# Performance work log

Measured on AMD Instinct MI355X. Metric: run time of the kernel, lower is better.

Reference implementation:

```python
import math
import jax, jax.numpy as jnp
import numpy as np

N_HEAD = 16
ROPE_BASE = 10000.0


def _qk_norm(x, scale):
    # RMSNorm over head_dim, eps added inside sqrt as in the torch code
    norm = jnp.sqrt(jnp.mean(x.astype(jnp.float32) ** 2, axis=-1, keepdims=True) + 1e-6)
    return (x.astype(jnp.float32) / norm * scale).astype(x.dtype)


def _rope3d(q, k, coords, token_type):
    # q,k: [B,H,T,D]; coords: [B,T,3]; token_type: [B,T]
    # head_dim is split into 3 equal chunks, chunk i rotated by coords[...,i].
    # Tokens with token_type == 0 (e.g. text tokens) are left unrotated.
    B, H, T, D = q.shape
    d3 = D // 3
    half = d3 // 2
    inv_freq = ROPE_BASE ** (-jnp.arange(half, dtype=jnp.float32) / half)  # [half]

    def rotate(x):
        # x: [B,H,T,D] -> rotate each of the 3 axis-chunks
        chunks = []
        for a in range(3):
            xa = x[..., a * d3:(a + 1) * d3]                       # [B,H,T,d3]
            ang = coords[:, None, :, a, None] * inv_freq            # [B,1,T,half]
            cos, sin = jnp.cos(ang), jnp.sin(ang)
            x1, x2 = xa[..., :half], xa[..., half:]
            chunks.append(jnp.concatenate([x1 * cos - x2 * sin,
                                           x1 * sin + x2 * cos], axis=-1))
        rot = jnp.concatenate(chunks, axis=-1)
        apply = (token_type > 0)[:, None, :, None]                  # [B,1,T,1]
        return jnp.where(apply, rot, x)

    return rotate(q), rotate(k)


def setup_inputs() -> dict:
    key = jax.random.key(0)
    ks = jax.random.split(key, 5)
    B, T, C = 2, 2048, 1536
    D = C // N_HEAD
    return {
        "x": jax.random.normal(ks[0], (B, T, C), jnp.float32),
        "coords": jax.random.uniform(ks[1], (B, T, 3), jnp.float32) * 32.0,
        "token_type": jax.random.randint(ks[2], (B, T), 0, 2),
        "W_qkv": jax.random.normal(ks[3], (3 * C, C), jnp.float32) * (1.0 / math.sqrt(C)),
        "W_out": jax.random.normal(ks[4], (C, C), jnp.float32) * (1.0 / math.sqrt(C)),
        "q_scale": jnp.ones((D,), jnp.float32),
        "k_scale": jnp.ones((D,), jnp.float32),
    }


def reference(x, coords, token_type, W_qkv, W_out, q_scale, k_scale):
    B, T, C = x.shape
    H = N_HEAD
    D = C // H
    qkv = x @ W_qkv.T                                   # [B,T,3C]
    q, k, v = jnp.split(qkv, 3, axis=-1)
    q = q.reshape(B, T, H, D).transpose(0, 2, 1, 3)     # [B,H,T,D]
    k = k.reshape(B, T, H, D).transpose(0, 2, 1, 3)
    v = v.reshape(B, T, H, D).transpose(0, 2, 1, 3)
    q = _qk_norm(q, q_scale)
    k = _qk_norm(k, k_scale)
    q, k = _rope3d(q, k, coords, token_type)
    scale = 1.0 / math.sqrt(D)
    attn = jnp.einsum('bhqd,bhkd->bhqk', q, k) * scale  # [B,H,T,T]
    causal = jnp.tril(jnp.ones((T, T), bool))
    attn = jnp.where(causal, attn, -jnp.inf)
    attn = jax.nn.softmax(attn, axis=-1)
    out = jnp.einsum('bhqk,bhkd->bhqd', attn, v)        # [B,H,T,D]
    out = out.transpose(0, 2, 1, 3).reshape(B, T, C)
    return out @ W_out.T
```

## Files before the change

### kernel.cpp

```cpp
#include <hip/hip_runtime.h>
#include <stdint.h>
#include <stddef.h>


typedef __attribute__((ext_vector_type(8))) __bf16 bf16x8;
typedef __attribute__((ext_vector_type(4))) __bf16 bf16x4;
typedef __attribute__((ext_vector_type(4))) float  f32x4;

#define NB 2
#define NT 2048
#define NC 1536
#define NH 16
#define ND 96
#define NQKV 4608
#define NM 4096

static __device__ __forceinline__ float fexp2(float x) {
#if __has_builtin(__builtin_amdgcn_exp2f)
  return __builtin_amdgcn_exp2f(x);
#else
  return exp2f(x);
#endif
}

static __device__ __forceinline__ void g2lds16(const void* g, void* l) {
  __builtin_amdgcn_global_load_lds(
      (const __attribute__((address_space(1))) void*)g,
      (__attribute__((address_space(3))) void*)l, 16, 0, 0);
}

__global__ __launch_bounds__(256) void cvt_f32_bf16(
    const float4* __restrict__ src, bf16x4* __restrict__ dst, int n4) {
  int i = blockIdx.x * 256 + threadIdx.x;
  if (i < n4) {
    float4 v = src[i];
    bf16x4 o;
    o[0] = (__bf16)v.x; o[1] = (__bf16)v.y;
    o[2] = (__bf16)v.z; o[3] = (__bf16)v.w;
    dst[i] = o;
  }
}

#define BAR1() do { __builtin_amdgcn_s_barrier(); \
                    asm volatile("" ::: "memory"); } while (0)
#define BAR2() do { asm volatile("" ::: "memory"); \
                    __builtin_amdgcn_s_barrier(); } while (0)
#define WAITLGKM() do { asm volatile("s_waitcnt lgkmcnt(0)" ::: "memory"); \
                        __builtin_amdgcn_sched_barrier(0); } while (0)
#define WAITVM6() asm volatile("s_waitcnt vmcnt(6)" ::: "memory")
#define WAITVM5() asm volatile("s_waitcnt vmcnt(5)" ::: "memory")

template <int MH>
static __device__ __forceinline__ void readA2(
    bf16x8 (&aR)[2][2], const char* buf, int aro, int sk0, int sk1) {
#pragma unroll
  for (int i = 0; i < 2; ++i) {
    const char* p = buf + aro + (MH * 2 + i) * 2048;
    aR[i][0] = *(const bf16x8*)(p + sk0);
    aR[i][1] = *(const bf16x8*)(p + sk1);
  }
}
template <int NF0, int NN>
static __device__ __forceinline__ void readBN(
    bf16x8 (&bb)[NN][2], const char* buf, int bro, int sk0, int sk1) {
#pragma unroll
  for (int j = 0; j < NN; ++j) {
    const char* p = buf + bro + (NF0 + j) * 2048;
    bb[j][0] = *(const bf16x8*)(p + sk0);
    bb[j][1] = *(const bf16x8*)(p + sk1);
  }
}
template <int MH, int NF0, int NN>
static __device__ __forceinline__ void quadN(
    f32x4 (&acc)[4][9], const bf16x8 (&aR)[2][2], const bf16x8 (&bb)[NN][2]) {
  __builtin_amdgcn_s_setprio(1);
#pragma unroll
  for (int i = 0; i < 2; ++i)
#pragma unroll
    for (int j = 0; j < NN; ++j)
#pragma unroll
      for (int ks = 0; ks < 2; ++ks)
        acc[MH * 2 + i][NF0 + j] = __builtin_amdgcn_mfma_f32_16x16x32_bf16(
            aR[i][ks], bb[j][ks], acc[MH * 2 + i][NF0 + j], 0, 0, 0);
  __builtin_amdgcn_s_setprio(0);
}

__global__ __launch_bounds__(512, 2) void gemm1_8ph(
    const __bf16* __restrict__ A, const __bf16* __restrict__ Bw,
    __bf16* __restrict__ C, int M, int N, int K) {
  __shared__ __align__(16) char lds[139264];
  char* const A0 = lds;
  char* const A1 = lds + 32768;
  char* const B0 = lds + 65536;
  char* const B1 = lds + 102400;

  const int tid = threadIdx.x;
  const int l   = tid & 63;
  const int w   = tid >> 6;
  const int wm  = w >> 1;
  const int wn  = w & 1;
  const int lm  = l & 15;
  const int lq  = l >> 4;

  const int nnt = 16;
  const int nwg = gridDim.x * gridDim.y;
  const int lid = blockIdx.y * gridDim.x + blockIdx.x;
  const int swz = (lid & 7) * (nwg >> 3) + (lid >> 3);
  const int m0  = (swz / nnt) * 256;
  const int n0  = (swz % nnt) * 288;

  const int aro = (wm * 64 + lm) * 128;
  const int bro = (wn * 144 + lm) * 128;
  const int sk0 = ((lq) ^ (lm & 7)) * 16;
  const int sk1 = ((4 + lq) ^ (lm & 7)) * 16;

  const int ssl = ((l & 7) ^ ((l >> 3) & 7)) * 8;
  auto stageA = [&](int grow0, int k0, char* dst) {
#pragma unroll
    for (int q2 = 0; q2 < 2; ++q2) {
      const int c   = w * 2 + q2;
      const int row = c * 8 + (l >> 3);
      g2lds16(A + (size_t)(grow0 + row) * K + k0 + ssl, dst + c * 1024);
    }
  };
  auto stageB = [&](int grow0, int k0, char* dst) {
#pragma unroll
    for (int q2 = 0; q2 < 2; ++q2) {
      const int c   = w * 2 + q2;
      const int row = c * 8 + (l >> 3);
      g2lds16(Bw + (size_t)(grow0 + row) * K + k0 + ssl, dst + c * 1024);
    }
    if (w < 2) {
      const int c   = 16 + w;
      const int row = c * 8 + (l >> 3);
      g2lds16(Bw + (size_t)(grow0 + row) * K + k0 + ssl, dst + c * 1024);
    }
  };

  f32x4 acc[4][9] = {};
  bf16x8 aL[2][2], aH[2][2], b5[5][2], b4[4][2];

  stageA(m0,       0,  A0);
  stageA(m0 + 128, 0,  A0 + 16384);
  stageB(n0,       0,  B0);
  stageB(n0 + 144, 0,  B0 + 18432);
  stageA(m0,       64, A1);
  stageA(m0 + 128, 64, A1 + 16384);

  const int NIT = K >> 7;
  for (int it = 0; it < NIT; ++it) {
    const int kh  = it * 128 + 64;
    const int knl = it * 128 + 128;
    const int knh = it * 128 + 192;
    stageB(n0, kh, B1);
    WAITVM6();
    BAR1();
    readA2<0>(aL, A0, aro, sk0, sk1);
    readBN<0, 5>(b5, B0, bro, sk0, sk1);
    WAITLGKM();
    quadN<0, 0, 5>(acc, aL, b5);
    BAR2();
    stageB(n0 + 144, kh, B1 + 18432);
    BAR1();
    readA2<1>(aH, A0, aro, sk0, sk1);
    WAITLGKM();
    quadN<1, 0, 5>(acc, aH, b5);
    BAR2();
    stageA(m0, knl, A0);
    BAR1();
    readBN<5, 4>(b4, B0, bro, sk0, sk1);
    WAITLGKM();
    quadN<1, 5, 4>(acc, aH, b4);
    BAR2();
    stageA(m0 + 128, knl, A0 + 16384);
    BAR1();
    quadN<0, 5, 4>(acc, aL, b4);
    BAR2();
    stageB(n0, knl, B0);
    WAITVM6();
    BAR1();
    readA2<0>(aL, A1, aro, sk0, sk1);
    readBN<0, 5>(b5, B1, bro, sk0, sk1);
    WAITLGKM();
    quadN<0, 0, 5>(acc, aL, b5);
    BAR2();
    stageB(n0 + 144, knl, B0 + 18432);
    BAR1();
    readA2<1>(aH, A1, aro, sk0, sk1);
    WAITLGKM();
    quadN<1, 0, 5>(acc, aH, b5);
    BAR2();
    stageA(m0, knh, A1);
    BAR1();
    readBN<5, 4>(b4, B1, bro, sk0, sk1);
    WAITLGKM();
    quadN<1, 5, 4>(acc, aH, b4);
    BAR2();
    stageA(m0 + 128, knh, A1 + 16384);
    BAR1();
    quadN<0, 5, 4>(acc, aL, b4);
    BAR2();
  }

  const int r0 = lq * 4;
#pragma unroll
  for (int mf = 0; mf < 4; ++mf)
#pragma unroll
    for (int nf = 0; nf < 9; ++nf)
#pragma unroll
      for (int r = 0; r < 4; ++r) {
        const size_t row = (size_t)(m0 + wm * 64 + mf * 16 + r0 + r);
        const size_t col = (size_t)(n0 + wn * 144 + nf * 16 + lm);
        C[row * N + col] = (__bf16)acc[mf][nf][r];
      }
}

template <int MH>
static __device__ __forceinline__ void g2readA(
    bf16x8 (&aR)[2][2], const char* buf, int aro, int sk0, int sk1) {
#pragma unroll
  for (int i = 0; i < 2; ++i) {
    const char* p = buf + aro + (MH * 2 + i) * 2048;
    aR[i][0] = *(const bf16x8*)(p + sk0);
    aR[i][1] = *(const bf16x8*)(p + sk1);
  }
}
template <int NF0, int NN>
static __device__ __forceinline__ void g2readB(
    bf16x8 (&bb)[NN][2], const char* buf, int bro, int sk0, int sk1) {
#pragma unroll
  for (int j = 0; j < NN; ++j) {
    const char* p = buf + bro + (NF0 + j) * 2048;
    bb[j][0] = *(const bf16x8*)(p + sk0);
    bb[j][1] = *(const bf16x8*)(p + sk1);
  }
}
template <int MH, int NF0, int NN>
static __device__ __forceinline__ void g2quad(
    f32x4 (&acc)[4][3], const bf16x8 (&aR)[2][2], const bf16x8 (&bb)[NN][2]) {
  __builtin_amdgcn_s_setprio(1);
#pragma unroll
  for (int i = 0; i < 2; ++i)
#pragma unroll
    for (int j = 0; j < NN; ++j)
#pragma unroll
      for (int ks = 0; ks < 2; ++ks)
        acc[MH * 2 + i][NF0 + j] = __builtin_amdgcn_mfma_f32_16x16x32_bf16(
            aR[i][ks], bb[j][ks], acc[MH * 2 + i][NF0 + j], 0, 0, 0);
  __builtin_amdgcn_s_setprio(0);
}

__global__ __launch_bounds__(512, 2) void gemm2_8ph(
    const __bf16* __restrict__ A, const __bf16* __restrict__ Bw,
    float* __restrict__ C, int M, int N, int K) {
  __shared__ __align__(16) char lds[81920];
  char* const A0 = lds;
  char* const A1 = lds + 16384;
  char* const B0 = lds + 32768;
  char* const B1 = lds + 57344;

  const int tid = threadIdx.x;
  const int l   = tid & 63;
  const int w   = tid >> 6;
  const int wm  = w >> 2;
  const int wn  = w & 3;
  const int lm  = l & 15;
  const int lq  = l >> 4;

  const int nwg = gridDim.x * gridDim.y;
  const int lid = blockIdx.y * gridDim.x + blockIdx.x;
  const int swz = (lid & 7) * (nwg >> 3) + (lid >> 3);
  const int m0  = (swz / 8) * 128;
  const int n0  = (swz % 8) * 192;

  const int aro = (wm * 64 + lm) * 128;
  const int bro = (wn * 48 + lm) * 128;
  const int sk0 = ((lq) ^ (lm & 7)) * 16;
  const int sk1 = ((4 + lq) ^ (lm & 7)) * 16;

  const int ssl = ((l & 7) ^ ((l >> 3) & 7)) * 8;
  auto stageA = [&](int k0, char* dst) {
#pragma unroll
    for (int q2 = 0; q2 < 2; ++q2) {
      const int c   = w * 2 + q2;
      const int row = c * 8 + (l >> 3);
      g2lds16(A + (size_t)(m0 + row) * K + k0 + ssl, dst + c * 1024);
    }
  };
  auto stageB = [&](int k0, char* dst) {
#pragma unroll
    for (int q2 = 0; q2 < 3; ++q2) {
      const int c   = w * 3 + q2;
      const int row = c * 8 + (l >> 3);
      g2lds16(Bw + (size_t)(n0 + row) * K + k0 + ssl, dst + c * 1024);
    }
  };

  f32x4 acc[4][3] = {};
  bf16x8 aL[2][2], aH[2][2], bL[2][2], bH[1][2];

  stageA(0,  A0);
  stageB(0,  B0);
  stageA(64, A1);

  const int NIT = K >> 7;
  for (int it = 0; it < NIT; ++it) {
    const int kh  = it * 128 + 64;
    const int knl = it * 128 + 128;
    const int knh = it * 128 + 192;
    stageB(kh, B1);
    WAITVM5();
    BAR1();
    g2readA<0>(aL, A0, aro, sk0, sk1);
    g2readB<0, 2>(bL, B0, bro, sk0, sk1);
    WAITLGKM();
    g2quad<0, 0, 2>(acc, aL, bL);
    BAR2();
    BAR1();
    g2readA<1>(aH, A0, aro, sk0, sk1);
    WAITLGKM();
    g2quad<1, 0, 2>(acc, aH, bL);
    BAR2();
    stageA(knl, A0);
    BAR1();
    g2readB<2, 1>(bH, B0, bro, sk0, sk1);
    WAITLGKM();
    g2quad<1, 2, 1>(acc, aH, bH);
    BAR2();
    BAR1();
    g2quad<0, 2, 1>(acc, aL, bH);
    BAR2();
    stageB(knl, B0);
    WAITVM5();
    BAR1();
    g2readA<0>(aL, A1, aro, sk0, sk1);
    g2readB<0, 2>(bL, B1, bro, sk0, sk1);
    WAITLGKM();
    g2quad<0, 0, 2>(acc, aL, bL);
    BAR2();
    BAR1();
    g2readA<1>(aH, A1, aro, sk0, sk1);
    WAITLGKM();
    g2quad<1, 0, 2>(acc, aH, bL);
    BAR2();
    stageA(knh, A1);
    BAR1();
    g2readB<2, 1>(bH, B1, bro, sk0, sk1);
    WAITLGKM();
    g2quad<1, 2, 1>(acc, aH, bH);
    BAR2();
    BAR1();
    g2quad<0, 2, 1>(acc, aL, bH);
    BAR2();
  }

  const int r0 = lq * 4;
#pragma unroll
  for (int mf = 0; mf < 4; ++mf)
#pragma unroll
    for (int nf = 0; nf < 3; ++nf)
#pragma unroll
      for (int r = 0; r < 4; ++r) {
        const size_t row = (size_t)(m0 + wm * 64 + mf * 16 + r0 + r);
        const size_t col = (size_t)(n0 + wn * 48 + nf * 16 + lm);
        C[row * N + col] = acc[mf][nf][r];
      }
}

static __device__ __forceinline__ float rope_one(float v, float p, int d,
                                                 const float* c3) {
  const int a  = d >> 5;
  const int j  = d & 31;
  const int jj = j & 15;
  const float invf = fexp2((float)jj * -0.8304820237218406f);
  const float ang  = c3[a] * invf;
  float sn, cs;
  __sincosf(ang, &sn, &cs);
  return (j < 16) ? (v * cs - p * sn) : (v * cs + p * sn);
}

__global__ __launch_bounds__(256) void normrope_kernel(
    const __bf16* __restrict__ qkv, const float* __restrict__ coords,
    const int* __restrict__ ttype, const float* __restrict__ qsc,
    const float* __restrict__ ksc, __bf16* __restrict__ qo,
    __bf16* __restrict__ ko) {
  const int l   = threadIdx.x & 63;
  const int w   = threadIdx.x >> 6;
  const int rid = blockIdx.x * 4 + w;
  const int h   = rid & (NH - 1);
  const int bt  = rid >> 4;
  const int t   = bt & (NT - 1);
  const int b   = bt >> 11;
  const __bf16* base = qkv + (size_t)bt * NQKV + h * ND;
  const float*  c3   = coords + (size_t)bt * 3;
  const bool rope    = ttype[bt] > 0;
  const size_t bh    = (size_t)(b * NH + h);

  {
    float x0 = (float)base[l];
    float x1 = (l < 32) ? (float)base[64 + l] : 0.f;
    float ss = x0 * x0 + x1 * x1;
#pragma unroll
    for (int off = 1; off < 64; off <<= 1) ss += __shfl_xor(ss, off, 64);
    const float rn = rsqrtf(ss * (1.f / 96.f) + 1e-6f);
    x0 *= rn * qsc[l];
    if (l < 32) x1 *= rn * qsc[64 + l];
    const float p0 = __shfl_xor(x0, 16, 64);
    const float p1 = __shfl_xor(x1, 16, 64);
    if (rope) {
      x0 = rope_one(x0, p0, l, c3);
      if (l < 32) x1 = rope_one(x1, p1, 64 + l, c3);
    }
    __bf16* dst = qo + (bh * NT + t) * ND;
    dst[l] = (__bf16)x0;
    if (l < 32) dst[64 + l] = (__bf16)x1;
  }
  {
    float x0 = (float)base[NC + l];
    float x1 = (l < 32) ? (float)base[NC + 64 + l] : 0.f;
    float ss = x0 * x0 + x1 * x1;
#pragma unroll
    for (int off = 1; off < 64; off <<= 1) ss += __shfl_xor(ss, off, 64);
    const float rn = rsqrtf(ss * (1.f / 96.f) + 1e-6f);
    x0 *= rn * ksc[l];
    if (l < 32) x1 *= rn * ksc[64 + l];
    const float p0 = __shfl_xor(x0, 16, 64);
    const float p1 = __shfl_xor(x1, 16, 64);
    if (rope) {
      x0 = rope_one(x0, p0, l, c3);
      if (l < 32) x1 = rope_one(x1, p1, 64 + l, c3);
    }
    __bf16* dst = ko + (bh * NT + t) * ND;
    dst[l] = (__bf16)x0;
    if (l < 32) dst[64 + l] = (__bf16)x1;
  }
}

__global__ __launch_bounds__(256) void transpose_v(
    const __bf16* __restrict__ qkv, __bf16* __restrict__ vo) {
  __shared__ __align__(16) __bf16 tile[96][264];
  const int tid = threadIdx.x;
  const int bh  = blockIdx.y;
  const int t0  = blockIdx.x * 256;
  const int b   = bh >> 4, h = bh & 15;
  const __bf16* src =
      qkv + ((size_t)(b * NT + t0 + tid)) * NQKV + 2 * NC + h * ND;
#pragma unroll
  for (int ch = 0; ch < 12; ++ch) {
    bf16x8 v = *(const bf16x8*)(src + ch * 8);
#pragma unroll
    for (int j = 0; j < 8; ++j) tile[ch * 8 + j][tid] = v[j];
  }
  __syncthreads();
#pragma unroll
  for (int k = 0; k < 12; ++k) {
    const int c  = tid + k * 256;
    const int d  = c >> 5;
    const int tc = c & 31;
    bf16x8 v = *(const bf16x8*)(&tile[d][tc * 8]);
    *(bf16x8*)(vo + ((size_t)bh * ND + d) * NT + t0 + tc * 8) = v;
  }
}

static __device__ __forceinline__ void attn_tile(
    const bf16x8 (&aq)[3], const bf16x8 (&bk)[2][3], int q0r, int n0,
    int lm, int lq, f32x4& lsum, __bf16* pbase ) {
  f32x4 s[2];
#pragma unroll
  for (int nt = 0; nt < 2; ++nt) {
    f32x4 a = {};
#pragma unroll
    for (int c = 0; c < 3; ++c)
      a = __builtin_amdgcn_mfma_f32_16x16x32_bf16(aq[c], bk[nt][c], a, 0, 0, 0);
    s[nt] = a;
  }
  if (n0 + 31 > q0r) {
#pragma unroll
    for (int nt = 0; nt < 2; ++nt)
#pragma unroll
      for (int r = 0; r < 4; ++r)
        if (n0 + nt * 16 + lm > q0r + lq * 4 + r) s[nt][r] = -1e30f;
  }
  const float cl = 0.10206207261596575f * 1.4426950408889634f;
#pragma unroll
  for (int nt = 0; nt < 2; ++nt)
#pragma unroll
    for (int r = 0; r < 4; ++r)
      s[nt][r] = fexp2((s[nt][r] - 96.0f) * cl);
#pragma unroll
  for (int r = 0; r < 4; ++r) lsum[r] += s[0][r] + s[1][r];
#pragma unroll
  for (int nt = 0; nt < 2; ++nt)
#pragma unroll
    for (int r = 0; r < 4; ++r)
      pbase[(lq * 4 + r) * 40 + nt * 16 + lm] = (__bf16)s[nt][r];
}

__global__ __launch_bounds__(512) void attn_fwd2(
    const __bf16* __restrict__ q, const __bf16* __restrict__ k,
    const __bf16* __restrict__ vt, __bf16* __restrict__ out) {
  __shared__ __align__(16) char KV[2][12288];
  __shared__ __align__(16) __bf16 plds[8][2][16][40];
  const int tid = threadIdx.x;
  const int l   = tid & 63;
  const int w   = tid >> 6;
  const int bh  = blockIdx.y;
  const int qp  = blockIdx.x;
  const int lm  = l & 15;
  const int lq  = l >> 4;
  const int q0L = qp * 128 + w * 16;
  const int q0H = (15 - qp) * 128 + w * 16;
  const int nktLw = qp * 4 + (w >> 1) + 1;
  const int nktHw = (15 - qp) * 4 + (w >> 1) + 1;
  const int nkt   = (15 - qp) * 4 + 4;
  const __bf16* qh = q  + (size_t)bh * NT * ND;
  const __bf16* kh = k  + (size_t)bh * NT * ND;
  const __bf16* vh = vt + (size_t)bh * ND * NT;
  __bf16* pbL = &plds[w][0][0][0];
  __bf16* pbH = &plds[w][1][0][0];

  auto stage = [&](int n0, char* buf) {
    if (w < 6) {
      const int nt = w / 3, c = w - nt * 3;
      g2lds16(kh + (size_t)(n0 + nt * 16 + (l >> 2)) * ND + c * 32 + (l & 3) * 8,
              buf + w * 1024);
    } else {
      const int v = w - 6;
      g2lds16(vh + (size_t)(v * 16 + (l >> 2)) * NT + n0 + (l & 3) * 8,
              buf + 6144 + v * 1024);
    }
    if (w < 4) {
      const int v = 2 + w;
      g2lds16(vh + (size_t)(v * 16 + (l >> 2)) * NT + n0 + (l & 3) * 8,
              buf + 6144 + v * 1024);
    }
  };

  bf16x8 aqL[3], aqH[3];
#pragma unroll
  for (int c = 0; c < 3; ++c) {
    aqL[c] = *(const bf16x8*)(qh + (size_t)(q0L + lm) * ND + c * 32 + lq * 8);
    aqH[c] = *(const bf16x8*)(qh + (size_t)(q0H + lm) * ND + c * 32 + lq * 8);
  }

  f32x4 oL[6] = {}, oH[6] = {};
  f32x4 lsL = {}, lsH = {};
  const int ji = (lm * 4 + lq) * 16;

  stage(0, KV[0]);
  for (int kt = 0; kt < nkt; ++kt) {
    __syncthreads();
    if (kt + 1 < nkt) stage((kt + 1) * 32, KV[(kt + 1) & 1]);
    const char* Kc = KV[kt & 1];
    const char* Vc = KV[kt & 1] + 6144;
    const int n0 = kt * 32;
    bf16x8 bk[2][3];
#pragma unroll
    for (int nt = 0; nt < 2; ++nt)
#pragma unroll
      for (int c = 0; c < 3; ++c)
        bk[nt][c] = *(const bf16x8*)(Kc + (nt * 3 + c) * 1024 + ji);
    const bool doL = kt < nktLw;
    const bool doH = kt < nktHw;
    if (doL) attn_tile(aqL, bk, q0L, n0, lm, lq, lsL, pbL);
    if (doH) attn_tile(aqH, bk, q0H, n0, lm, lq, lsH, pbH);
    bf16x8 apL = {}, apH = {};
    if (doL) apL = *(const bf16x8*)(pbL + lm * 40 + lq * 8);
    if (doH) apH = *(const bf16x8*)(pbH + lm * 40 + lq * 8);
#pragma unroll
    for (int dt = 0; dt < 6; ++dt) {
      bf16x8 bv = *(const bf16x8*)(Vc + dt * 1024 + ji);
      if (doL) oL[dt] = __builtin_amdgcn_mfma_f32_16x16x32_bf16(apL, bv, oL[dt], 0, 0, 0);
      if (doH) oH[dt] = __builtin_amdgcn_mfma_f32_16x16x32_bf16(apH, bv, oH[dt], 0, 0, 0);
    }
  }

  const int b = bh >> 4, h = bh & 15;
#pragma unroll
  for (int f = 0; f < 2; ++f) {
    const f32x4* o = f ? oH : oL;
    const f32x4& ls = f ? lsH : lsL;
    const int q0 = f ? q0H : q0L;
    float rl[4];
#pragma unroll
    for (int r = 0; r < 4; ++r) {
      float v = ls[r];
#pragma unroll
      for (int off = 1; off < 16; off <<= 1) v += __shfl_xor(v, off, 64);
      rl[r] = 1.f / v;
    }
#pragma unroll
    for (int dt = 0; dt < 6; ++dt)
#pragma unroll
      for (int r = 0; r < 4; ++r) {
        const int t = q0 + lq * 4 + r;
        out[((size_t)(b * NT + t)) * NC + h * ND + dt * 16 + lm] =
            (__bf16)(o[dt][r] * rl[r]);
      }
  }
}

static constexpr size_t OFF_XB   = 0;
static constexpr size_t OFF_WQKV = 12582912;
static constexpr size_t OFF_WOUT = 26738688;
static constexpr size_t OFF_QKV  = 31457280;
static constexpr size_t OFF_Q    = 69206016;
static constexpr size_t OFF_K    = 81788928;
static constexpr size_t OFF_VT   = 94371840;

extern "C" void kernel_launch(void* const* d_in, const int* in_sizes, int n_in,
                              void* d_out, int out_size, void* d_ws,
                              size_t ws_size, hipStream_t stream) {
  const float* x      = (const float*)d_in[0];
  const float* coords = (const float*)d_in[1];
  const int*   ttype  = (const int*)d_in[2];
  const float* wqkv   = (const float*)d_in[3];
  const float* wout   = (const float*)d_in[4];
  const float* qs     = (const float*)d_in[5];
  const float* ks     = (const float*)d_in[6];

  char* ws = (char*)d_ws;
  __bf16* xb    = (__bf16*)(ws + OFF_XB);
  __bf16* wqkvb = (__bf16*)(ws + OFF_WQKV);
  __bf16* woutb = (__bf16*)(ws + OFF_WOUT);
  __bf16* qkvb  = (__bf16*)(ws + OFF_QKV);
  __bf16* qb    = (__bf16*)(ws + OFF_Q);
  __bf16* kb    = (__bf16*)(ws + OFF_K);
  __bf16* vtb   = (__bf16*)(ws + OFF_VT);
  __bf16* attnb = (__bf16*)(ws + OFF_XB);

  {
    const int n4x = NM * NC / 4;
    const int n4w = NQKV * NC / 4;
    const int n4o = NC * NC / 4;
    cvt_f32_bf16<<<(n4x + 255) / 256, 256, 0, stream>>>(
        (const float4*)x, (bf16x4*)xb, n4x);
    cvt_f32_bf16<<<(n4w + 255) / 256, 256, 0, stream>>>(
        (const float4*)wqkv, (bf16x4*)wqkvb, n4w);
    cvt_f32_bf16<<<(n4o + 255) / 256, 256, 0, stream>>>(
        (const float4*)wout, (bf16x4*)woutb, n4o);
  }
  gemm1_8ph<<<dim3(NQKV / 288, NM / 256), 512, 0, stream>>>(
      xb, wqkvb, qkvb, NM, NQKV, NC);
  normrope_kernel<<<(NB * NT * NH) / 4, 256, 0, stream>>>(
      qkvb, coords, ttype, qs, ks, qb, kb);
  transpose_v<<<dim3(NT / 256, NB * NH), 256, 0, stream>>>(qkvb, vtb);
  attn_fwd2<<<dim3(8, NB * NH), 512, 0, stream>>>(qb, kb, vtb, attnb);
  gemm2_8ph<<<dim3(NC / 192, NM / 128), 512, 0, stream>>>(
      attnb, woutb, (float*)d_out, NM, NC, NC);
}
```

Baseline: 304.9 us.

## Reorder GEMM LDS reads before staging and widen attention KV tiles to 64 keys

In both GEMM kernels, the LDS fragment reads now come before the next global-to-LDS stage. The vmcnt waits move to the end of each half-iteration, so loads overlap compute with fewer barriers per stage. The attention kernel now processes 64-key tiles instead of 32, doubling the KV shared buffer and the P scratch. This halves the number of loop iterations and block-wide syncs per tile. The costs are more LDS use, which may lower occupancy, and coarser causal masking work on diagonal tiles.

Result: slower. 311.1 us (+2.1%).

```diff
diff --git a/kernel.cpp b/kernel.cpp
--- a/kernel.cpp
+++ b/kernel.cpp
@@ -47,8 +47,8 @@
                     __builtin_amdgcn_s_barrier(); } while (0)
 #define WAITLGKM() do { asm volatile("s_waitcnt lgkmcnt(0)" ::: "memory"); \
                         __builtin_amdgcn_sched_barrier(0); } while (0)
-#define WAITVM6() asm volatile("s_waitcnt vmcnt(6)" ::: "memory")
-#define WAITVM5() asm volatile("s_waitcnt vmcnt(5)" ::: "memory")
+#define WAITVM4() asm volatile("s_waitcnt vmcnt(4)" ::: "memory")
+#define WAITVM2() asm volatile("s_waitcnt vmcnt(2)" ::: "memory")
 
 template <int MH>
 static __device__ __forceinline__ void readA2(
@@ -146,59 +146,61 @@
   stageB(n0 + 144, 0,  B0 + 18432);
   stageA(m0,       64, A1);
   stageA(m0 + 128, 64, A1 + 16384);
+  WAITVM4();
+  __builtin_amdgcn_s_barrier();
 
   const int NIT = K >> 7;
   for (int it = 0; it < NIT; ++it) {
     const int kh  = it * 128 + 64;
     const int knl = it * 128 + 128;
     const int knh = it * 128 + 192;
-    stageB(n0, kh, B1);
-    WAITVM6();
-    BAR1();
     readA2<0>(aL, A0, aro, sk0, sk1);
     readBN<0, 5>(b5, B0, bro, sk0, sk1);
+    stageB(n0, kh, B1);
+    BAR1();
     WAITLGKM();
     quadN<0, 0, 5>(acc, aL, b5);
     BAR2();
+    readA2<1>(aH, A0, aro, sk0, sk1);
     stageB(n0 + 144, kh, B1 + 18432);
     BAR1();
-    readA2<1>(aH, A0, aro, sk0, sk1);
     WAITLGKM();
     quadN<1, 0, 5>(acc, aH, b5);
     BAR2();
+    readBN<5, 4>(b4, B0, bro, sk0, sk1);
     stageA(m0, knl, A0);
     BAR1();
-    readBN<5, 4>(b4, B0, bro, sk0, sk1);
     WAITLGKM();
     quadN<1, 5, 4>(acc, aH, b4);
     BAR2();
     stageA(m0 + 128, knl, A0 + 16384);
     BAR1();
     quadN<0, 5, 4>(acc, aL, b4);
-    BAR2();
-    stageB(n0, knl, B0);
-    WAITVM6();
-    BAR1();
+    WAITVM4();
+    BAR2();
     readA2<0>(aL, A1, aro, sk0, sk1);
     readBN<0, 5>(b5, B1, bro, sk0, sk1);
+    stageB(n0, knl, B0);
+    BAR1();
     WAITLGKM();
     quadN<0, 0, 5>(acc, aL, b5);
     BAR2();
+    readA2<1>(aH, A1, aro, sk0, sk1);
     stageB(n0 + 144, knl, B0 + 18432);
     BAR1();
-    readA2<1>(aH, A1, aro, sk0, sk1);
     WAITLGKM();
     quadN<1, 0, 5>(acc, aH, b5);
     BAR2();
+    readBN<5, 4>(b4, B1, bro, sk0, sk1);
     stageA(m0, knh, A1);
     BAR1();
-    readBN<5, 4>(b4, B1, bro, sk0, sk1);
     WAITLGKM();
     quadN<1, 5, 4>(acc, aH, b4);
     BAR2();
     stageA(m0 + 128, knh, A1 + 16384);
     BAR1();
     quadN<0, 5, 4>(acc, aL, b4);
+    WAITVM4();
     BAR2();
   }
 
@@ -215,26 +217,6 @@
       }
 }
 
-template <int MH>
-static __device__ __forceinline__ void g2readA(
-    bf16x8 (&aR)[2][2], const char* buf, int aro, int sk0, int sk1) {
-#pragma unroll
-  for (int i = 0; i < 2; ++i) {
-    const char* p = buf + aro + (MH * 2 + i) * 2048;
-    aR[i][0] = *(const bf16x8*)(p + sk0);
-    aR[i][1] = *(const bf16x8*)(p + sk1);
-  }
-}
-template <int NF0, int NN>
-static __device__ __forceinline__ void g2readB(
-    bf16x8 (&bb)[NN][2], const char* buf, int bro, int sk0, int sk1) {
-#pragma unroll
-  for (int j = 0; j < NN; ++j) {
-    const char* p = buf + bro + (NF0 + j) * 2048;
-    bb[j][0] = *(const bf16x8*)(p + sk0);
-    bb[j][1] = *(const bf16x8*)(p + sk1);
-  }
-}
 template <int MH, int NF0, int NN>
 static __device__ __forceinline__ void g2quad(
     f32x4 (&acc)[4][3], const bf16x8 (&aR)[2][2], const bf16x8 (&bb)[NN][2]) {
@@ -302,55 +284,57 @@
   stageA(0,  A0);
   stageB(0,  B0);
   stageA(64, A1);
+  WAITVM2();
+  __builtin_amdgcn_s_barrier();
 
   const int NIT = K >> 7;
   for (int it = 0; it < NIT; ++it) {
     const int kh  = it * 128 + 64;
     const int knl = it * 128 + 128;
     const int knh = it * 128 + 192;
+    readA2<0>(aL, A0, aro, sk0, sk1);
+    readBN<0, 2>(bL, B0, bro, sk0, sk1);
     stageB(kh, B1);
-    WAITVM5();
-    BAR1();
-    g2readA<0>(aL, A0, aro, sk0, sk1);
-    g2readB<0, 2>(bL, B0, bro, sk0, sk1);
+    BAR1();
     WAITLGKM();
     g2quad<0, 0, 2>(acc, aL, bL);
     BAR2();
-    BAR1();
-    g2readA<1>(aH, A0, aro, sk0, sk1);
+    readA2<1>(aH, A0, aro, sk0, sk1);
+    BAR1();
     WAITLGKM();
     g2quad<1, 0, 2>(acc, aH, bL);
     BAR2();
+    readBN<2, 1>(bH, B0, bro, sk0, sk1);
     stageA(knl, A0);
     BAR1();
-    g2readB<2, 1>(bH, B0, bro, sk0, sk1);
     WAITLGKM();
     g2quad<1, 2, 1>(acc, aH, bH);
     BAR2();
     BAR1();
     g2quad<0, 2, 1>(acc, aL, bH);
-    BAR2();
+    WAITVM2();
+    BAR2();
+    readA2<0>(aL, A1, aro, sk0, sk1);
+    readBN<0, 2>(bL, B1, bro, sk0, sk1);
     stageB(knl, B0);
-    WAITVM5();
-    BAR1();
-    g2readA<0>(aL, A1, aro, sk0, sk1);
-    g2readB<0, 2>(bL, B1, bro, sk0, sk1);
+    BAR1();
     WAITLGKM();
     g2quad<0, 0, 2>(acc, aL, bL);
     BAR2();
-    BAR1();
-    g2readA<1>(aH, A1, aro, sk0, sk1);
+    readA2<1>(aH, A1, aro, sk0, sk1);
+    BAR1();
     WAITLGKM();
     g2quad<1, 0, 2>(acc, aH, bL);
     BAR2();
+    readBN<2, 1>(bH, B1, bro, sk0, sk1);
     stageA(knh, A1);
     BAR1();
-    g2readB<2, 1>(bH, B1, bro, sk0, sk1);
     WAITLGKM();
     g2quad<1, 2, 1>(acc, aH, bH);
     BAR2();
     BAR1();
     g2quad<0, 2, 1>(acc, aL, bH);
+    WAITVM2();
     BAR2();
   }
 
@@ -462,45 +446,47 @@
   }
 }
 
-static __device__ __forceinline__ void attn_tile(
-    const bf16x8 (&aq)[3], const bf16x8 (&bk)[2][3], int q0r, int n0,
+static __device__ __forceinline__ void attn_tile64(
+    const bf16x8 (&aq)[3], const bf16x8 (&bk)[4][3], int q0r, int n0,
     int lm, int lq, f32x4& lsum, __bf16* pbase ) {
-  f32x4 s[2];
-#pragma unroll
-  for (int nt = 0; nt < 2; ++nt) {
+  f32x4 s[4];
+#pragma unroll
+  for (int nt = 0; nt < 4; ++nt) {
     f32x4 a = {};
 #pragma unroll
     for (int c = 0; c < 3; ++c)
       a = __builtin_amdgcn_mfma_f32_16x16x32_bf16(aq[c], bk[nt][c], a, 0, 0, 0);
     s[nt] = a;
   }
-  if (n0 + 31 > q0r) {
-#pragma unroll
-    for (int nt = 0; nt < 2; ++nt)
+  if (n0 + 63 > q0r) {
+#pragma unroll
+    for (int nt = 0; nt < 4; ++nt)
 #pragma unroll
       for (int r = 0; r < 4; ++r)
         if (n0 + nt * 16 + lm > q0r + lq * 4 + r) s[nt][r] = -1e30f;
   }
   const float cl = 0.10206207261596575f * 1.4426950408889634f;
 #pragma unroll
-  for (int nt = 0; nt < 2; ++nt)
+  for (int nt = 0; nt < 4; ++nt)
 #pragma unroll
     for (int r = 0; r < 4; ++r)
       s[nt][r] = fexp2((s[nt][r] - 96.0f) * cl);
 #pragma unroll
-  for (int r = 0; r < 4; ++r) lsum[r] += s[0][r] + s[1][r];
-#pragma unroll
-  for (int nt = 0; nt < 2; ++nt)
+  for (int r = 0; r < 4; ++r)
+    lsum[r] += (s[0][r] + s[1][r]) + (s[2][r] + s[3][r]);
+#pragma unroll
+  for (int nt = 0; nt < 4; ++nt)
 #pragma unroll
     for (int r = 0; r < 4; ++r)
-      pbase[(lq * 4 + r) * 40 + nt * 16 + lm] = (__bf16)s[nt][r];
+      pbase[(nt >> 1) * 640 + (lq * 4 + r) * 40 + (nt & 1) * 16 + lm] =
+          (__bf16)s[nt][r];
 }
 
 __global__ __launch_bounds__(512) void attn_fwd2(
     const __bf16* __restrict__ q, const __bf16* __restrict__ k,
     const __bf16* __restrict__ vt, __bf16* __restrict__ out) {
-  __shared__ __align__(16) char KV[2][12288];
-  __shared__ __align__(16) __bf16 plds[8][2][16][40];
+  __shared__ __align__(16) char KV[2][24576];
+  __shared__ __align__(16) __bf16 plds[8][2][2][16][40];
   const int tid = threadIdx.x;
   const int l   = tid & 63;
   const int w   = tid >> 6;
@@ -510,29 +496,29 @@
   const int lq  = l >> 4;
   const int q0L = qp * 128 + w * 16;
   const int q0H = (15 - qp) * 128 + w * 16;
-  const int nktLw = qp * 4 + (w >> 1) + 1;
-  const int nktHw = (15 - qp) * 4 + (w >> 1) + 1;
-  const int nkt   = (15 - qp) * 4 + 4;
+  const int nktLw = qp * 2 + (w >> 2) + 1;
+  const int nktHw = (15 - qp) * 2 + (w >> 2) + 1;
+  const int nkt   = (15 - qp) * 2 + 2;
   const __bf16* qh = q  + (size_t)bh * NT * ND;
   const __bf16* kh = k  + (size_t)bh * NT * ND;
   const __bf16* vh = vt + (size_t)bh * ND * NT;
-  __bf16* pbL = &plds[w][0][0][0];
-  __bf16* pbH = &plds[w][1][0][0];
+  __bf16* pbL = &plds[w][0][0][0][0];
+  __bf16* pbH = &plds[w][1][0][0][0];
 
   auto stage = [&](int n0, char* buf) {
-    if (w < 6) {
-      const int nt = w / 3, c = w - nt * 3;
-      g2lds16(kh + (size_t)(n0 + nt * 16 + (l >> 2)) * ND + c * 32 + (l & 3) * 8,
-              buf + w * 1024);
-    } else {
-      const int v = w - 6;
-      g2lds16(vh + (size_t)(v * 16 + (l >> 2)) * NT + n0 + (l & 3) * 8,
-              buf + 6144 + v * 1024);
-    }
-    if (w < 4) {
-      const int v = 2 + w;
-      g2lds16(vh + (size_t)(v * 16 + (l >> 2)) * NT + n0 + (l & 3) * 8,
-              buf + 6144 + v * 1024);
+#pragma unroll
+    for (int q2 = 0; q2 < 3; ++q2) {
+      const int g = w * 3 + q2;
+      if (g < 12) {
+        const int nt = g / 3, c = g - nt * 3;
+        g2lds16(kh + (size_t)(n0 + nt * 16 + (l >> 2)) * ND + c * 32 + (l & 3) * 8,
+                buf + g * 1024);
+      } else {
+        const int gv = g - 12;
+        const int dt = gv >> 1, hf = gv & 1;
+        g2lds16(vh + (size_t)(dt * 16 + (l >> 2)) * NT + n0 + hf * 32 + (l & 3) * 8,
+                buf + 12288 + gv * 1024);
+      }
     }
   };
 
@@ -550,28 +536,41 @@
   stage(0, KV[0]);
   for (int kt = 0; kt < nkt; ++kt) {
     __syncthreads();
-    if (kt + 1 < nkt) stage((kt + 1) * 32, KV[(kt + 1) & 1]);
+    if (kt + 1 < nkt) stage((kt + 1) * 64, KV[(kt + 1) & 1]);
     const char* Kc = KV[kt & 1];
-    const char* Vc = KV[kt & 1] + 6144;
-    const int n0 = kt * 32;
-    bf16x8 bk[2][3];
-#pragma unroll
-    for (int nt = 0; nt < 2; ++nt)
+    const char* Vc = KV[kt & 1] + 12288;
+    const int n0 = kt * 64;
+    bf16x8 bk[4][3];
+#pragma unroll
+    for (int nt = 0; nt < 4; ++nt)
 #pragma unroll
       for (int c = 0; c < 3; ++c)
         bk[nt][c] = *(const bf16x8*)(Kc + (nt * 3 + c) * 1024 + ji);
     const bool doL = kt < nktLw;
     const bool doH = kt < nktHw;
-    if (doL) attn_tile(aqL, bk, q0L, n0, lm, lq, lsL, pbL);
-    if (doH) attn_tile(aqH, bk, q0H, n0, lm, lq, lsH, pbH);
-    bf16x8 apL = {}, apH = {};
-    if (doL) apL = *(const bf16x8*)(pbL + lm * 40 + lq * 8);
-    if (doH) apH = *(const bf16x8*)(pbH + lm * 40 + lq * 8);
+    if (doL) attn_tile64(aqL, bk, q0L, n0, lm, lq, lsL, pbL);
+    if (doH) attn_tile64(aqH, bk, q0H, n0, lm, lq, lsH, pbH);
+    bf16x8 apL0 = {}, apL1 = {}, apH0 = {}, apH1 = {};
+    if (doL) {
+      apL0 = *(const bf16x8*)(pbL + lm * 40 + lq * 8);
+      apL1 = *(const bf16x8*)(pbL + 640 + lm * 40 + lq * 8);
+    }
+    if (doH) {
+      apH0 = *(const bf16x8*)(pbH + lm * 40 + lq * 8);
+      apH1 = *(const bf16x8*)(pbH + 640 + lm * 40 + lq * 8);
+    }
 #pragma unroll
     for (int dt = 0; dt < 6; ++dt) {
-      bf16x8 bv = *(const bf16x8*)(Vc + dt * 1024 + ji);
-      if (doL) oL[dt] = __builtin_amdgcn_mfma_f32_16x16x32_bf16(apL, bv, oL[dt], 0, 0, 0);
-      if (doH) oH[dt] = __builtin_amdgcn_mfma_f32_16x16x32_bf16(apH, bv, oH[dt], 0, 0, 0);
+      bf16x8 bv0 = *(const bf16x8*)(Vc + (dt * 2 + 0) * 1024 + ji);
+      bf16x8 bv1 = *(const bf16x8*)(Vc + (dt * 2 + 1) * 1024 + ji);
+      if (doL) {
+        oL[dt] = __builtin_amdgcn_mfma_f32_16x16x32_bf16(apL0, bv0, oL[dt], 0, 0, 0);
+        oL[dt] = __builtin_amdgcn_mfma_f32_16x16x32_bf16(apL1, bv1, oL[dt], 0, 0, 0);
+      }
+      if (doH) {
+        oH[dt] = __builtin_amdgcn_mfma_f32_16x16x32_bf16(apH0, bv0, oH[dt], 0, 0, 0);
+        oH[dt] = __builtin_amdgcn_mfma_f32_16x16x32_bf16(apH1, bv1, oH[dt], 0, 0, 0);
+      }
     }
   }
 
```
